# Performance work log

Hardware: AMD Instinct MI355X
Metric: run time of the kernel (lower is better)

The kernel has to match this reference:

```python
import jax, jax.numpy as jnp
import numpy as np

N_EMBD = 1024
N_HEAD = 16
HEAD = N_EMBD // N_HEAD
B, T = 4, 2048


def setup_inputs() -> dict:
    key = jax.random.key(0)
    ks = jax.random.split(key, 9)
    s = 1.0 / np.sqrt(N_EMBD)
    return {
        "x": jax.random.normal(ks[0], (B, T, N_EMBD), dtype=jnp.float32),
        "Wk": jax.random.uniform(ks[1], (N_EMBD, N_EMBD), jnp.float32, -s, s),
        "bk": jax.random.uniform(ks[2], (N_EMBD,), jnp.float32, -s, s),
        "Wq": jax.random.uniform(ks[3], (N_EMBD, N_EMBD), jnp.float32, -s, s),
        "bq": jax.random.uniform(ks[4], (N_EMBD,), jnp.float32, -s, s),
        "Wv": jax.random.uniform(ks[5], (N_EMBD, N_EMBD), jnp.float32, -s, s),
        "bv": jax.random.uniform(ks[6], (N_EMBD,), jnp.float32, -s, s),
        "Wp": jax.random.uniform(ks[7], (N_EMBD, N_EMBD), jnp.float32, -s, s),
        "bp": jax.random.uniform(ks[8], (N_EMBD,), jnp.float32, -s, s),
    }


def reference(x, Wk, bk, Wq, bq, Wv, bv, Wp, bp):
    b, t, c = x.shape
    # torch Linear: y = x @ W.T + b
    def heads(W, bias):
        return (x @ W.T + bias).reshape(b, t, N_HEAD, HEAD).transpose(0, 2, 1, 3)
    k = heads(Wk, bk)  # [B,H,T,D]
    q = heads(Wq, bq)
    v = heads(Wv, bv)
    att = jnp.einsum("bhqd,bhkd->bhqk", q, k) * (1.0 / np.sqrt(HEAD))
    causal = jnp.tril(jnp.ones((t, t), dtype=bool))
    att = jnp.where(causal, att, -jnp.inf)
    att = jax.nn.softmax(att, axis=-1)
    y = jnp.einsum("bhqk,bhkd->bhqd", att, v)  # [B,H,T,D]
    y = y.transpose(0, 2, 1, 3).reshape(b, t, c)
    return y @ Wp.T + bp
```

## Files before the change

kernel.cpp:

```cpp
#include <hip/hip_runtime.h>
#include <stdint.h>

typedef short bf16x8 __attribute__((ext_vector_type(8)));
typedef float f32x4 __attribute__((ext_vector_type(4)));
typedef float f32x16 __attribute__((ext_vector_type(16)));

#define MFMA16(a, b, c) __builtin_amdgcn_mfma_f32_16x16x32_bf16((a), (b), (c), 0, 0, 0)
#define MFMA32(a, b, c) __builtin_amdgcn_mfma_f32_32x32x16_bf16((a), (b), (c), 0, 0, 0)

__device__ __forceinline__ unsigned short f2bf(float x) {
  union { float f; unsigned int u; } v; v.f = x;
  unsigned int r = (v.u + 0x7FFFu + ((v.u >> 16) & 1u)) >> 16;
  return (unsigned short)r;
}

__device__ __forceinline__ unsigned int cvtpk(float lo, float hi) {
  unsigned int r;
  asm("v_cvt_pk_bf16_f32 %0, %1, %2" : "=v"(r) : "v"(lo), "v"(hi));
  return r;
}

__device__ __forceinline__ void plswap(unsigned int& a, unsigned int& b) {
  asm("v_permlane32_swap_b32 %0, %1" : "+v"(a), "+v"(b));
}

__device__ __forceinline__ float exp2f_fast(float x) {
  float r;
  asm("v_exp_f32 %0, %1" : "=v"(r) : "v"(x));
  return r;
}

__global__ void __launch_bounds__(256) cvt_all(const float* __restrict__ x,
                                               const float* __restrict__ Wk,
                                               const float* __restrict__ Wq,
                                               const float* __restrict__ Wv,
                                               const float* __restrict__ Wp,
                                               unsigned short* __restrict__ xb,
                                               unsigned short* __restrict__ wqkvb,
                                               unsigned short* __restrict__ wpb) {
  const int stride = gridDim.x * blockDim.x;
  for (int i = blockIdx.x * blockDim.x + threadIdx.x; i < 3145728; i += stride) {
    if (i < 2097152) {
      float4 v = ((const float4*)x)[i];
      ushort4 o;
      o.x = f2bf(v.x); o.y = f2bf(v.y); o.z = f2bf(v.z); o.w = f2bf(v.w);
      ((ushort4*)xb)[i] = o;
      continue;
    }
    int j = i - 2097152;
    int sec = j >> 18;
    int off = j & 262143;
    const float4* s4 = (const float4*)(sec == 0 ? Wk : sec == 1 ? Wq : sec == 2 ? Wv : Wp);
    float4 v = s4[off];
    ushort4 o;
    o.x = f2bf(v.x); o.y = f2bf(v.y); o.z = f2bf(v.z); o.w = f2bf(v.w);
    if (sec < 3) ((ushort4*)wqkvb)[j] = o;
    else ((ushort4*)wpb)[off] = o;
  }
}

__global__ void __launch_bounds__(512) gemm_qkv8(const unsigned short* __restrict__ A,
                                                 const unsigned short* __restrict__ Bw,
                                                 const float* __restrict__ b0,
                                                 const float* __restrict__ b1,
                                                 const float* __restrict__ b2,
                                                 unsigned short* __restrict__ O0,
                                                 unsigned short* __restrict__ O1,
                                                 unsigned short* __restrict__ O2) {
  extern __shared__ unsigned short lds[];
#define HBASE(buf, isB, kk) \
  (lds + ((isB) ? (32768 + (buf)*12288 + (kk)*6144) : ((buf)*16384 + (kk)*8192)))

  const int tid = threadIdx.x;
  const int wid = tid >> 6;
  const int l = tid & 63;
  const int g = l >> 4;
  const int ln = l & 15;

  const int bid = blockIdx.x;
  const int swz = (bid & 7) * 64 + (bid >> 3);
  const int bx = swz & 15;
  const int by = swz >> 4;
  const int m0 = by * 256;
  const int n0 = bx * 192;
  const int wm = (wid >> 2) * 128;
  const int wn = (wid & 3) * 48;

  f32x4 acc[8][3];
#pragma unroll
  for (int i = 0; i < 8; ++i)
#pragma unroll
    for (int j = 0; j < 3; ++j) acc[i][j] = (f32x4){0.f, 0.f, 0.f, 0.f};

#define STAGEA(buf, kk, kt)                                                                       \
  {                                                                                               \
    unsigned short* dst = HBASE(buf, 0, kk);                                                      \
    _Pragma("unroll") for (int i = 0; i < 2; ++i) {                                               \
      int c = i * 512 + tid;                                                                      \
      int r = c >> 2;                                                                             \
      int x = (c & 3) ^ ((r >> 1) & 3);                                                           \
      const unsigned short* gp = A + (size_t)(m0 + r) * 1024 + (kt) + (kk)*32 + x * 8;            \
      __builtin_amdgcn_global_load_lds((const __attribute__((address_space(1))) void*)gp,         \
                                       (__attribute__((address_space(3))) void*)&dst[c * 8],      \
                                       16, 0, 0);                                                 \
    }                                                                                             \
  }
#define STAGEB(buf, kk, kt)                                                                       \
  {                                                                                               \
    unsigned short* dst = HBASE(buf, 1, kk);                                                      \
    _Pragma("unroll") for (int i = 0; i < 2; ++i) {                                               \
      int c = (i == 0) ? tid : (512 + (tid & 255));                                               \
      int r = c >> 2;                                                                             \
      int x = (c & 3) ^ ((r >> 1) & 3);                                                           \
      const unsigned short* gp = Bw + (size_t)(n0 + r) * 1024 + (kt) + (kk)*32 + x * 8;           \
      __builtin_amdgcn_global_load_lds((const __attribute__((address_space(1))) void*)gp,         \
                                       (__attribute__((address_space(3))) void*)&dst[c * 8],      \
                                       16, 0, 0);                                                 \
    }                                                                                             \
  }

  STAGEA(0, 0, 0);
  STAGEB(0, 0, 0);
  STAGEA(0, 1, 0);
  STAGEB(0, 1, 0);

  for (int T = 0; T < 16; ++T) {
    const int buf = T & 1;
    const int last = (T == 15);
    bf16x8 bF[3];
#pragma unroll
    for (int ph = 0; ph < 4; ++ph) {
      const int kk = ph >> 1;
      const int mg = ph & 1;

      if (mg == 0) {
        if (!last) asm volatile("s_waitcnt vmcnt(4)" ::: "memory");
        else asm volatile("s_waitcnt vmcnt(0)" ::: "memory");
      }
      if (!last) {
        if (ph == 0) STAGEA(buf ^ 1, 0, (T + 1) * 64);
        if (ph == 1) STAGEB(buf ^ 1, 0, (T + 1) * 64);
        if (ph == 2) STAGEA(buf ^ 1, 1, (T + 1) * 64);
        if (ph == 3) STAGEB(buf ^ 1, 1, (T + 1) * 64);
      }
      if (mg == 0) {
        __builtin_amdgcn_sched_barrier(0);
        __builtin_amdgcn_s_barrier();
        __builtin_amdgcn_sched_barrier(0);
#pragma unroll
        for (int ni = 0; ni < 3; ++ni) {
          int rb = wn + ni * 16 + ln;
          bF[ni] = *(const bf16x8*)&HBASE(buf, 1, kk)[rb * 32 + (g ^ ((rb >> 1) & 3)) * 8];
        }
      }
      bf16x8 aF[4];
#pragma unroll
      for (int j = 0; j < 4; ++j) {
        int ra = wm + (mg * 4 + j) * 16 + ln;
        aF[j] = *(const bf16x8*)&HBASE(buf, 0, kk)[ra * 32 + (g ^ ((ra >> 1) & 3)) * 8];
      }
      __builtin_amdgcn_s_setprio(1);
#pragma unroll
      for (int j = 0; j < 4; ++j)
#pragma unroll
        for (int ni = 0; ni < 3; ++ni)
          acc[mg * 4 + j][ni] = MFMA16(aF[j], bF[ni], acc[mg * 4 + j][ni]);
      __builtin_amdgcn_s_setprio(0);
      if (ph == 3) {
        __builtin_amdgcn_sched_barrier(0);
        __builtin_amdgcn_s_barrier();
        __builtin_amdgcn_sched_barrier(0);
      }
    }
  }
#undef STAGEA
#undef STAGEB
#undef HBASE

  const int mBase = m0 + wm + g * 4;
  const int nBase = n0 + wn + ln;
#pragma unroll
  for (int mi = 0; mi < 8; ++mi) {
    int mg2 = mBase + mi * 16;
    int b = mg2 >> 11, t = mg2 & 2047;
#pragma unroll
    for (int ni = 0; ni < 3; ++ni) {
      int n = nBase + ni * 16;
      int sec = n >> 10;
      int nn = n & 1023;
      int h = nn >> 6, d = nn & 63;
      const float* bias = (sec == 0) ? b0 : (sec == 1) ? b1 : b2;
      float bvl = bias[nn];
      if (sec == 2) {
        ushort4 pk;
        pk.x = f2bf(acc[mi][ni][0] + bvl);
        pk.y = f2bf(acc[mi][ni][1] + bvl);
        pk.z = f2bf(acc[mi][ni][2] + bvl);
        pk.w = f2bf(acc[mi][ni][3] + bvl);
        *(ushort4*)&O2[((size_t)((b * 16 + h) * 64 + d)) * 2048 + t] = pk;
      } else {
        unsigned short* O = sec ? O1 : O0;
        const float sc = sec ? (0.125f * 1.44269504f) : 1.0f;
#pragma unroll
        for (int r = 0; r < 4; ++r)
          O[((size_t)(b * 16 + h) * 2048 + (t + r)) * 64 + d] = f2bf((acc[mi][ni][r] + bvl) * sc);
      }
    }
  }
}

template <int MODE, int NX, int CPX>
__global__ void __launch_bounds__(512) gemm_big(const unsigned short* __restrict__ A,
                                                const unsigned short* __restrict__ Bw,
                                                const float* __restrict__ b0,
                                                float* __restrict__ Of) {
  extern __shared__ unsigned short lds[];

  const int tid = threadIdx.x;
  const int wid = tid >> 6;
  const int l = tid & 63;
  const int g = l >> 4;
  const int ln = l & 15;

  const int bid = blockIdx.x;
  const int swz = (bid & 7) * CPX + (bid >> 3);
  const int bx = swz % NX;
  const int by = swz / NX;
  const int m0 = by * 256;
  const int n0 = bx * 128;
  const int wm = (wid >> 1) * 64;
  const int wn = (wid & 1) * 64;

  f32x4 acc[4][4];
#pragma unroll
  for (int i = 0; i < 4; ++i)
#pragma unroll
    for (int j = 0; j < 4; ++j) acc[i][j] = (f32x4){0.f, 0.f, 0.f, 0.f};

#define STAGE_G(bufi, kt)                                                                         \
  {                                                                                               \
    unsigned short* Ad = lds + (bufi)*16384;                                                      \
    unsigned short* Bd = lds + 32768 + (bufi)*8192;                                               \
    _Pragma("unroll") for (int i = 0; i < 4; ++i) {                                               \
      int c = i * 512 + tid;                                                                      \
      int row = c >> 3;                                                                           \
      int cs = (c & 7) ^ (row & 7);                                                               \
      const unsigned short* ga = A + (size_t)(m0 + row) * 1024 + (kt) + cs * 8;                   \
      __builtin_amdgcn_global_load_lds((const __attribute__((address_space(1))) void*)ga,         \
                                       (__attribute__((address_space(3))) void*)&Ad[c * 8],       \
                                       16, 0, 0);                                                 \
    }                                                                                             \
    _Pragma("unroll") for (int i = 0; i < 2; ++i) {                                               \
      int c = i * 512 + tid;                                                                      \
      int row = c >> 3;                                                                           \
      int cs = (c & 7) ^ (row & 7);                                                               \
      const unsigned short* gb = Bw + (size_t)(n0 + row) * 1024 + (kt) + cs * 8;                  \
      __builtin_amdgcn_global_load_lds((const __attribute__((address_space(1))) void*)gb,         \
                                       (__attribute__((address_space(3))) void*)&Bd[c * 8],       \
                                       16, 0, 0);                                                 \
    }                                                                                             \
  }

  STAGE_G(0, 0);
  __syncthreads();

  for (int T = 0; T < 16; ++T) {
    const int buf = T & 1;
    if (T < 15) STAGE_G(buf ^ 1, (T + 1) * 64);

    const unsigned short* Ar = lds + buf * 16384;
    const unsigned short* Br = lds + 32768 + buf * 8192;
#pragma unroll
    for (int kk = 0; kk < 2; ++kk) {
      bf16x8 af[4], bfr[4];
#pragma unroll
      for (int mi = 0; mi < 4; ++mi) {
        int ra = wm + mi * 16 + ln;
        af[mi] = *(const bf16x8*)&Ar[ra * 64 + (((kk << 2) + g) ^ (ra & 7)) * 8];
      }
#pragma unroll
      for (int ni = 0; ni < 4; ++ni) {
        int rb = wn + ni * 16 + ln;
        bfr[ni] = *(const bf16x8*)&Br[rb * 64 + (((kk << 2) + g) ^ (rb & 7)) * 8];
      }
      __builtin_amdgcn_s_setprio(1);
#pragma unroll
      for (int mi = 0; mi < 4; ++mi)
#pragma unroll
        for (int ni = 0; ni < 4; ++ni) acc[mi][ni] = MFMA16(af[mi], bfr[ni], acc[mi][ni]);
      __builtin_amdgcn_s_setprio(0);
    }
    __syncthreads();
  }
#undef STAGE_G

  const int mBase = m0 + wm + g * 4;
  const int nBase = n0 + wn + ln;
#pragma unroll
  for (int mi = 0; mi < 4; ++mi) {
    int mg = mBase + mi * 16;
#pragma unroll
    for (int ni = 0; ni < 4; ++ni) {
      int n = nBase + ni * 16;
      float bvl = b0[n];
#pragma unroll
      for (int r = 0; r < 4; ++r) Of[(size_t)(mg + r) * 1024 + n] = acc[mi][ni][r] + bvl;
    }
  }
}

__global__ void __launch_bounds__(512) attn_kernel(const unsigned short* __restrict__ Q,
                                                   const unsigned short* __restrict__ K,
                                                   const unsigned short* __restrict__ Vt,
                                                   unsigned short* __restrict__ Y) {
  __shared__ unsigned short Ks[2][64 * 64];
  __shared__ unsigned short Vs[2][64 * 64];

  const int tid = threadIdx.x;
  const int wid = tid >> 6;
  const int l = tid & 63;
  const int q32 = l & 31;
  const int hi = l >> 5;
  const int bh = blockIdx.x & 63;
  const int u = blockIdx.x >> 6;
  const int j = (u < 4) ? u : (11 - u);
  const int qblk = (wid < 4) ? (15 - j) : j;
  const int q0w = qblk * 128 + (wid & 3) * 32;
  const int NT = 2 * (15 - j) + 2;
  const int myNt = (q0w + 95) >> 6;

  const unsigned short* Qp = Q + (size_t)bh * 2048 * 64;
  const unsigned short* Kp = K + (size_t)bh * 2048 * 64;
  const unsigned short* Vp = Vt + (size_t)bh * 64 * 2048;
  const int b = bh >> 4, h = bh & 15;

  const int srow = tid >> 3;
  const int csw = (tid & 7) ^ (srow & 7);

  bf16x8 qf[4];
#pragma unroll
  for (int kk = 0; kk < 4; ++kk)
    qf[kk] = *(const bf16x8*)&Qp[(size_t)(q0w + q32) * 64 + kk * 16 + hi * 8];

  f32x16 o0, o1;
#pragma unroll
  for (int r = 0; r < 16; ++r) { o0[r] = 0.f; o1[r] = 0.f; }
  float m = -1e30f, lst = 0.f;

#define STAGE(bufi, kk0)                                                                        \
  {                                                                                             \
    const unsigned short* gk = Kp + (size_t)((kk0) + srow) * 64 + csw * 8;                      \
    const unsigned short* gv = Vp + (size_t)srow * 2048 + (kk0) + csw * 8;                      \
    __builtin_amdgcn_global_load_lds((const __attribute__((address_space(1))) void*)gk,         \
                                     (__attribute__((address_space(3))) void*)                  \
                                         &Ks[bufi][wid * 512],                                  \
                                     16, 0, 0);                                                 \
    __builtin_amdgcn_global_load_lds((const __attribute__((address_space(1))) void*)gv,         \
                                     (__attribute__((address_space(3))) void*)                  \
                                         &Vs[bufi][wid * 512],                                  \
                                     16, 0, 0);                                                 \
  }

  int buf = 0;
  STAGE(0, 0);
  __syncthreads();

  for (int t = 0; t < NT; ++t) {
    const int k0 = t * 64;
    if (t + 1 < NT) STAGE(buf ^ 1, k0 + 64);

    if (t < myNt) {
      const int xr = q32 & 7;
      f32x16 s0, s1;
#pragma unroll
      for (int r = 0; r < 16; ++r) { s0[r] = 0.f; s1[r] = 0.f; }
      __builtin_amdgcn_s_setprio(1);
#pragma unroll
      for (int kk = 0; kk < 4; ++kk) {
        bf16x8 kf0 = *(const bf16x8*)&Ks[buf][q32 * 64 + (((kk << 1) | hi) ^ xr) * 8];
        bf16x8 kf1 = *(const bf16x8*)&Ks[buf][(32 + q32) * 64 + (((kk << 1) | hi) ^ xr) * 8];
        s0 = MFMA32(kf0, qf[kk], s0);
        s1 = MFMA32(kf1, qf[kk], s1);
      }
      __builtin_amdgcn_s_setprio(0);

      if (k0 + 63 > q0w) {
        const int qg = q0w + q32;
#pragma unroll
        for (int r = 0; r < 16; ++r) {
          int kr = (r & 3) + 8 * (r >> 2) + 4 * hi;
          if (k0 + kr > qg) s0[r] = -1e30f;
          if (k0 + 32 + kr > qg) s1[r] = -1e30f;
        }
      }

      float pm = fmaxf(fmaxf(s0[0], s0[1]), s0[2]);
#pragma unroll
      for (int r = 3; r < 15; r += 3) pm = fmaxf(fmaxf(fmaxf(s0[r], s0[r + 1]), s0[r + 2]), pm);
      pm = fmaxf(pm, s0[15]);
#pragma unroll
      for (int r = 0; r < 15; r += 3) pm = fmaxf(fmaxf(fmaxf(s1[r], s1[r + 1]), s1[r + 2]), pm);
      pm = fmaxf(pm, s1[15]);
      pm = fmaxf(pm, __shfl_xor(pm, 32));

      if (__any(pm > m + 11.0f)) {
        float mn = fmaxf(m, pm);
        float sf = exp2f_fast(m - mn);
        m = mn;
        lst *= sf;
#pragma unroll
        for (int r = 0; r < 16; ++r) {
          float sb2 = __shfl(sf, (r & 3) + 8 * (r >> 2) + 4 * hi);
          o0[r] *= sb2;
          o1[r] *= sb2;
        }
      }
      float rs = 0.f;
#pragma unroll
      for (int r = 0; r < 16; ++r) { s0[r] = exp2f_fast(s0[r] - m); rs += s0[r]; }
#pragma unroll
      for (int r = 0; r < 16; ++r) { s1[r] = exp2f_fast(s1[r] - m); rs += s1[r]; }
      rs += __shfl_xor(rs, 32);
      lst += rs;

      union { unsigned int u[4]; bf16x8 v; } pa[4];
#pragma unroll
      for (int t2 = 0; t2 < 2; ++t2) {
        const f32x16& sv = t2 ? s1 : s0;
#pragma unroll
        for (int sl = 0; sl < 2; ++sl) {
          int base = sl * 8;
          unsigned int x0 = cvtpk(sv[base + 0], sv[base + 1]);
          unsigned int x1 = cvtpk(sv[base + 2], sv[base + 3]);
          unsigned int x2 = cvtpk(sv[base + 4], sv[base + 5]);
          unsigned int x3 = cvtpk(sv[base + 6], sv[base + 7]);
          plswap(x0, x2);
          plswap(x1, x3);
          int ksg = t2 * 2 + sl;
          pa[ksg].u[0] = x0; pa[ksg].u[1] = x1; pa[ksg].u[2] = x2; pa[ksg].u[3] = x3;
        }
      }

      __builtin_amdgcn_s_setprio(1);
#pragma unroll
      for (int ksg = 0; ksg < 4; ++ksg) {
        bf16x8 v0 = *(const bf16x8*)&Vs[buf][q32 * 64 + (((ksg << 1) | hi) ^ xr) * 8];
        bf16x8 v1 = *(const bf16x8*)&Vs[buf][(32 + q32) * 64 + (((ksg << 1) | hi) ^ xr) * 8];
        o0 = MFMA32(pa[ksg].v, v0, o0);
        o1 = MFMA32(pa[ksg].v, v1, o1);
      }
      __builtin_amdgcn_s_setprio(0);
    }

    __syncthreads();
    buf ^= 1;
  }

#pragma unroll
  for (int r = 0; r < 16; ++r) {
    int qsrc = (r & 3) + 8 * (r >> 2) + 4 * hi;
    int qg = q0w + qsrc;
    float lq = __shfl(lst, qsrc);
    float inv = 1.0f / lq;
    size_t rowb = (size_t)(b * 2048 + qg) * 1024 + h * 64;
    Y[rowb + q32] = f2bf(o0[r] * inv);
    Y[rowb + 32 + q32] = f2bf(o1[r] * inv);
  }
#undef STAGE
}

extern "C" void kernel_launch(void* const* d_in, const int* in_sizes, int n_in,
                              void* d_out, int out_size, void* d_ws, size_t ws_size,
                              hipStream_t stream) {
  const float* x = (const float*)d_in[0];
  const float* Wk = (const float*)d_in[1];
  const float* bk = (const float*)d_in[2];
  const float* Wq = (const float*)d_in[3];
  const float* bq = (const float*)d_in[4];
  const float* Wv = (const float*)d_in[5];
  const float* bv = (const float*)d_in[6];
  const float* Wp = (const float*)d_in[7];
  const float* bp = (const float*)d_in[8];
  float* out = (float*)d_out;

  char* ws = (char*)d_ws;
  unsigned short* xb    = (unsigned short*)(ws);
  unsigned short* wqkvb = (unsigned short*)(ws + 16777216);
  unsigned short* wpb   = (unsigned short*)(ws + 23068672);
  unsigned short* Qb    = (unsigned short*)(ws + 25165824);
  unsigned short* Kb    = (unsigned short*)(ws + 41943040);
  unsigned short* Vtb   = (unsigned short*)(ws + 58720256);
  unsigned short* yb    = (unsigned short*)(ws + 75497472);
  if (ws_size < 92274688u) return;

  const int LDS_Q = 114688;
  const int LDS_P = 98304;
  (void)hipFuncSetAttribute((const void*)&gemm_qkv8,
                            hipFuncAttributeMaxDynamicSharedMemorySize, LDS_Q);
  (void)hipFuncSetAttribute((const void*)&gemm_big<1, 8, 32>,
                            hipFuncAttributeMaxDynamicSharedMemorySize, LDS_P);

  cvt_all<<<dim3(3072), dim3(256), 0, stream>>>(x, Wk, Wq, Wv, Wp, xb, wqkvb, wpb);

  gemm_qkv8<<<dim3(512), dim3(512), LDS_Q, stream>>>(xb, wqkvb, bk, bq, bv, Kb, Qb, Vtb);

  attn_kernel<<<dim3(512), dim3(512), 0, stream>>>(Qb, Kb, Vtb, yb);

  gemm_big<1, 8, 32><<<dim3(256), dim3(512), LDS_P, stream>>>(yb, wpb, bp, out);
}
```

Before: 150.4 us.

## Restructure output projection GEMM with split-K halves, phased prefetch and fine waitcnts

Replaces the templated output-projection GEMM with a dedicated kernel. It splits each 64-wide K tile into two 32-wide LDS halves with a new XOR swizzle, and issues the next tile's loads in four phases interleaved with MFMA work, using explicit vmcnt waits and raw s_barrier instead of __syncthreads. The wave layout changes from 4x2 waves of 64x64 to 2x4 waves of 128x32. The aim is to overlap global-to-LDS loads with compute and cut barrier stalls in a small GEMM that is only one part of the total time. The hand-written waitcnt counts and barrier placement are fragile and could introduce races.

Result: no change. 151.3 us (+0.6%).

```diff
diff --git a/kernel.cpp b/kernel.cpp
--- a/kernel.cpp
+++ b/kernel.cpp
@@ -209,12 +209,13 @@
   }
 }
 
-template <int MODE, int NX, int CPX>
-__global__ void __launch_bounds__(512) gemm_big(const unsigned short* __restrict__ A,
-                                                const unsigned short* __restrict__ Bw,
-                                                const float* __restrict__ b0,
-                                                float* __restrict__ Of) {
+__global__ void __launch_bounds__(512) gemm_proj8(const unsigned short* __restrict__ A,
+                                                  const unsigned short* __restrict__ Bw,
+                                                  const float* __restrict__ b0,
+                                                  float* __restrict__ Of) {
   extern __shared__ unsigned short lds[];
+#define HBASE(buf, isB, kk) \
+  (lds + ((isB) ? (32768 + (buf)*8192 + (kk)*4096) : ((buf)*16384 + (kk)*8192)))
 
   const int tid = threadIdx.x;
   const int wid = tid >> 6;
@@ -223,88 +224,116 @@
   const int ln = l & 15;
 
   const int bid = blockIdx.x;
-  const int swz = (bid & 7) * CPX + (bid >> 3);
-  const int bx = swz % NX;
-  const int by = swz / NX;
+  const int swz = (bid & 7) * 32 + (bid >> 3);
+  const int bx = swz & 7;
+  const int by = swz >> 3;
   const int m0 = by * 256;
   const int n0 = bx * 128;
-  const int wm = (wid >> 1) * 64;
-  const int wn = (wid & 1) * 64;
-
-  f32x4 acc[4][4];
-#pragma unroll
-  for (int i = 0; i < 4; ++i)
-#pragma unroll
-    for (int j = 0; j < 4; ++j) acc[i][j] = (f32x4){0.f, 0.f, 0.f, 0.f};
-
-#define STAGE_G(bufi, kt)                                                                         \
+  const int wm = (wid >> 2) * 128;
+  const int wn = (wid & 3) * 32;
+
+  f32x4 acc[8][2];
+#pragma unroll
+  for (int i = 0; i < 8; ++i)
+#pragma unroll
+    for (int j = 0; j < 2; ++j) acc[i][j] = (f32x4){0.f, 0.f, 0.f, 0.f};
+
+#define STAGEA(buf, kk, kt)                                                                       \
   {                                                                                               \
-    unsigned short* Ad = lds + (bufi)*16384;                                                      \
-    unsigned short* Bd = lds + 32768 + (bufi)*8192;                                               \
-    _Pragma("unroll") for (int i = 0; i < 4; ++i) {                                               \
+    unsigned short* dst = HBASE(buf, 0, kk);                                                      \
+    _Pragma("unroll") for (int i = 0; i < 2; ++i) {                                               \
       int c = i * 512 + tid;                                                                      \
-      int row = c >> 3;                                                                           \
-      int cs = (c & 7) ^ (row & 7);                                                               \
-      const unsigned short* ga = A + (size_t)(m0 + row) * 1024 + (kt) + cs * 8;                   \
-      __builtin_amdgcn_global_load_lds((const __attribute__((address_space(1))) void*)ga,         \
-                                       (__attribute__((address_space(3))) void*)&Ad[c * 8],       \
+      int r = c >> 2;                                                                             \
+      int x = (c & 3) ^ ((r >> 1) & 3);                                                           \
+      const unsigned short* gp = A + (size_t)(m0 + r) * 1024 + (kt) + (kk)*32 + x * 8;            \
+      __builtin_amdgcn_global_load_lds((const __attribute__((address_space(1))) void*)gp,         \
+                                       (__attribute__((address_space(3))) void*)&dst[c * 8],      \
                                        16, 0, 0);                                                 \
     }                                                                                             \
-    _Pragma("unroll") for (int i = 0; i < 2; ++i) {                                               \
-      int c = i * 512 + tid;                                                                      \
-      int row = c >> 3;                                                                           \
-      int cs = (c & 7) ^ (row & 7);                                                               \
-      const unsigned short* gb = Bw + (size_t)(n0 + row) * 1024 + (kt) + cs * 8;                  \
-      __builtin_amdgcn_global_load_lds((const __attribute__((address_space(1))) void*)gb,         \
-                                       (__attribute__((address_space(3))) void*)&Bd[c * 8],       \
+  }
+#define STAGEB(buf, kk, kt)                                                                       \
+  {                                                                                               \
+    unsigned short* dst = HBASE(buf, 1, kk);                                                      \
+    {                                                                                             \
+      int c = tid;                                                                                \
+      int r = c >> 2;                                                                             \
+      int x = (c & 3) ^ ((r >> 1) & 3);                                                           \
+      const unsigned short* gp = Bw + (size_t)(n0 + r) * 1024 + (kt) + (kk)*32 + x * 8;           \
+      __builtin_amdgcn_global_load_lds((const __attribute__((address_space(1))) void*)gp,         \
+                                       (__attribute__((address_space(3))) void*)&dst[c * 8],      \
                                        16, 0, 0);                                                 \
     }                                                                                             \
   }
 
-  STAGE_G(0, 0);
-  __syncthreads();
+  STAGEA(0, 0, 0);
+  STAGEB(0, 0, 0);
+  STAGEA(0, 1, 0);
+  STAGEB(0, 1, 0);
 
   for (int T = 0; T < 16; ++T) {
     const int buf = T & 1;
-    if (T < 15) STAGE_G(buf ^ 1, (T + 1) * 64);
-
-    const unsigned short* Ar = lds + buf * 16384;
-    const unsigned short* Br = lds + 32768 + buf * 8192;
-#pragma unroll
-    for (int kk = 0; kk < 2; ++kk) {
-      bf16x8 af[4], bfr[4];
-#pragma unroll
-      for (int mi = 0; mi < 4; ++mi) {
-        int ra = wm + mi * 16 + ln;
-        af[mi] = *(const bf16x8*)&Ar[ra * 64 + (((kk << 2) + g) ^ (ra & 7)) * 8];
-      }
-#pragma unroll
-      for (int ni = 0; ni < 4; ++ni) {
-        int rb = wn + ni * 16 + ln;
-        bfr[ni] = *(const bf16x8*)&Br[rb * 64 + (((kk << 2) + g) ^ (rb & 7)) * 8];
+    const int last = (T == 15);
+    bf16x8 bF[2];
+#pragma unroll
+    for (int ph = 0; ph < 4; ++ph) {
+      const int kk = ph >> 1;
+      const int mg = ph & 1;
+
+      if (mg == 0) {
+        if (!last) asm volatile("s_waitcnt vmcnt(3)" ::: "memory");
+        else asm volatile("s_waitcnt vmcnt(0)" ::: "memory");
+      }
+      if (!last) {
+        if (ph == 0) STAGEA(buf ^ 1, 0, (T + 1) * 64);
+        if (ph == 1) STAGEB(buf ^ 1, 0, (T + 1) * 64);
+        if (ph == 2) STAGEA(buf ^ 1, 1, (T + 1) * 64);
+        if (ph == 3) STAGEB(buf ^ 1, 1, (T + 1) * 64);
+      }
+      if (mg == 0) {
+        __builtin_amdgcn_sched_barrier(0);
+        __builtin_amdgcn_s_barrier();
+        __builtin_amdgcn_sched_barrier(0);
+#pragma unroll
+        for (int ni = 0; ni < 2; ++ni) {
+          int rb = wn + ni * 16 + ln;
+          bF[ni] = *(const bf16x8*)&HBASE(buf, 1, kk)[rb * 32 + (g ^ ((rb >> 1) & 3)) * 8];
+        }
+      }
+      bf16x8 aF[4];
+#pragma unroll
+      for (int j = 0; j < 4; ++j) {
+        int ra = wm + (mg * 4 + j) * 16 + ln;
+        aF[j] = *(const bf16x8*)&HBASE(buf, 0, kk)[ra * 32 + (g ^ ((ra >> 1) & 3)) * 8];
       }
       __builtin_amdgcn_s_setprio(1);
 #pragma unroll
-      for (int mi = 0; mi < 4; ++mi)
-#pragma unroll
-        for (int ni = 0; ni < 4; ++ni) acc[mi][ni] = MFMA16(af[mi], bfr[ni], acc[mi][ni]);
+      for (int j = 0; j < 4; ++j)
+#pragma unroll
+        for (int ni = 0; ni < 2; ++ni)
+          acc[mg * 4 + j][ni] = MFMA16(aF[j], bF[ni], acc[mg * 4 + j][ni]);
       __builtin_amdgcn_s_setprio(0);
+      if (ph == 3) {
+        __builtin_amdgcn_sched_barrier(0);
+        __builtin_amdgcn_s_barrier();
+        __builtin_amdgcn_sched_barrier(0);
+      }
     }
-    __syncthreads();
-  }
-#undef STAGE_G
+  }
+#undef STAGEA
+#undef STAGEB
+#undef HBASE
 
   const int mBase = m0 + wm + g * 4;
   const int nBase = n0 + wn + ln;
 #pragma unroll
-  for (int mi = 0; mi < 4; ++mi) {
-    int mg = mBase + mi * 16;
-#pragma unroll
-    for (int ni = 0; ni < 4; ++ni) {
+  for (int mi = 0; mi < 8; ++mi) {
+    int mg2 = mBase + mi * 16;
+#pragma unroll
+    for (int ni = 0; ni < 2; ++ni) {
       int n = nBase + ni * 16;
       float bvl = b0[n];
 #pragma unroll
-      for (int r = 0; r < 4; ++r) Of[(size_t)(mg + r) * 1024 + n] = acc[mi][ni][r] + bvl;
+      for (int r = 0; r < 4; ++r) Of[(size_t)(mg2 + r) * 1024 + n] = acc[mi][ni][r] + bvl;
     }
   }
 }
@@ -497,7 +526,7 @@
   const int LDS_P = 98304;
   (void)hipFuncSetAttribute((const void*)&gemm_qkv8,
                             hipFuncAttributeMaxDynamicSharedMemorySize, LDS_Q);
-  (void)hipFuncSetAttribute((const void*)&gemm_big<1, 8, 32>,
+  (void)hipFuncSetAttribute((const void*)&gemm_proj8,
                             hipFuncAttributeMaxDynamicSharedMemorySize, LDS_P);
 
   cvt_all<<<dim3(3072), dim3(256), 0, stream>>>(x, Wk, Wq, Wv, Wp, xb, wqkvb, wpb);
@@ -506,5 +535,5 @@
 
   attn_kernel<<<dim3(512), dim3(512), 0, stream>>>(Qb, Kb, Vtb, yb);
 
-  gemm_big<1, 8, 32><<<dim3(256), dim3(512), LDS_P, stream>>>(yb, wpb, bp, out);
-}
+  gemm_proj8<<<dim3(256), dim3(512), LDS_P, stream>>>(yb, wpb, bp, out);
+}
```
